# Performance work log

Measured on AMD Instinct MI355X. Metric: run time of the kernel, lower is better.

The kernel has to match this reference:

```python
import jax, jax.numpy as jnp
import numpy as np

EMBED_DIM = 256
NUM_HEADS = 8
HEAD_DIM = EMBED_DIM // NUM_HEADS


def setup_inputs() -> dict:
    key = jax.random.key(0)
    ks = jax.random.split(key, 16)
    B, N, E = 4, 2048, EMBED_DIM
    s = 1.0 / np.sqrt(E)
    inp = {
        "x": jax.random.normal(ks[0], (B, N, E), jnp.float32),
        "influence_matrix": jax.random.uniform(ks[1], (B, N, N), jnp.float32),
        "Wq": jax.random.normal(ks[2], (E, E), jnp.float32) * s,
        "Wk": jax.random.normal(ks[3], (E, E), jnp.float32) * s,
        "Wv": jax.random.normal(ks[4], (E, E), jnp.float32) * s,
        "Wo": jax.random.normal(ks[5], (E, E), jnp.float32) * s,
        "bo": jnp.zeros((E,), jnp.float32),
        "iw1": jnp.array(1.0, jnp.float32),
        "ib1": jnp.array(0.0, jnp.float32),
        "iw2": jnp.array(1.0, jnp.float32),
        "ib2": jnp.array(0.0, jnp.float32),
        "W1": jax.random.normal(ks[6], (E, E), jnp.float32) * s,
        "b1": jnp.zeros((E,), jnp.float32),
        "W2": jax.random.normal(ks[7], (E, E), jnp.float32) * s,
        "b2": jnp.zeros((E,), jnp.float32),
        "g1": jnp.ones((E,), jnp.float32),
        "beta1": jnp.zeros((E,), jnp.float32),
        "g2": jnp.ones((E,), jnp.float32),
        "beta2": jnp.zeros((E,), jnp.float32),
    }
    return inp


def _layer_norm(x, g, b, eps=1e-5):
    mu = jnp.mean(x, axis=-1, keepdims=True)
    var = jnp.var(x, axis=-1, keepdims=True)
    return (x - mu) * jax.lax.rsqrt(var + eps) * g + b


def _attention(x, infl, Wq, Wk, Wv, Wo, bo, iw1, ib1, iw2, ib2):
    B, N, E = x.shape
    H, D = NUM_HEADS, HEAD_DIM
    # torch nn.Linear: y = x @ W.T ; here W is stored as (E, E) used directly.
    q = (x @ Wq).reshape(B, N, H, D)
    k = (x @ Wk).reshape(B, N, H, D)
    v = (x @ Wv).reshape(B, N, H, D)
    scores = jnp.einsum("bqhd,bkhd->bhqk", q, k) / np.sqrt(D)  # [B,H,N,N]
    scores = scores + (iw1 * infl + ib1)[:, None, :, :]
    w = jax.nn.softmax(scores, axis=-1)
    w = w * (iw2 * infl + ib2)[:, None, :, :]
    out = jnp.einsum("bhqk,bkhd->bqhd", w, v).reshape(B, N, E)
    return out @ Wo + bo


def reference(x, influence_matrix, Wq, Wk, Wv, Wo, bo, iw1, ib1, iw2, ib2,
              W1, b1, W2, b2, g1, beta1, g2, beta2):
    h = _attention(_layer_norm(x, g1, beta1), influence_matrix,
                   Wq, Wk, Wv, Wo, bo, iw1, ib1, iw2, ib2) + x
    ffn = jax.nn.relu(_layer_norm(h, g2, beta2) @ W1 + b1) @ W2 + b2
    return ffn + h
```

## Files before the change

### kernel.cpp

```cpp
#include <hip/hip_runtime.h>
#include <hip/hip_bf16.h>

#define B_  4
#define N_  2048
#define E_  256
#define H_  8
#define D_  32
#define QT  32
#define KC  64
#define HPB 4
#define VTP 72
#define PP  72
#define IFP 68
#define LOG2E 1.4426950408889634f

typedef __attribute__((ext_vector_type(8))) short bfx8;
typedef __attribute__((ext_vector_type(4))) float fx4;

__device__ __forceinline__ unsigned short f2bf(float f) {
    unsigned int u = __float_as_uint(f);
    u += 0x7fffu + ((u >> 16) & 1u);
    return (unsigned short)(u >> 16);
}

__device__ __forceinline__ float bf2f(unsigned short u) {
    return __uint_as_float((unsigned int)u << 16);
}

__device__ __forceinline__ unsigned int cvt_pk_bf16(float lo, float hi) {
    unsigned int r;
    asm("v_cvt_pk_bf16_f32 %0, %1, %2" : "=v"(r) : "v"(lo), "v"(hi));
    return r;
}

__global__ __launch_bounds__(256) void prep_w(
    const float* Wa, const float* Wb, const float* Wc,
    const float* Wd, const float* We, const float* Wf,
    unsigned short* Oa, unsigned short* Ob, unsigned short* Oc,
    unsigned short* Od, unsigned short* Oe, unsigned short* Of)
{
    int z = blockIdx.z;
    const float* src = z == 0 ? Wa : z == 1 ? Wb : z == 2 ? Wc
                     : z == 3 ? Wd : z == 4 ? We : Wf;
    unsigned short* dst = z == 0 ? Oa : z == 1 ? Ob : z == 2 ? Oc
                        : z == 3 ? Od : z == 4 ? Oe : Of;
    __shared__ float t[32][33];
    int n0 = blockIdx.x * 32, k0 = blockIdx.y * 32;
    int tx = threadIdx.x & 31, ty = threadIdx.x >> 5;
#pragma unroll
    for (int i = 0; i < 4; i++)
        t[ty + i * 8][tx] = src[(k0 + ty + i * 8) * E_ + n0 + tx];
    __syncthreads();
#pragma unroll
    for (int i = 0; i < 4; i++)
        dst[(n0 + ty + i * 8) * E_ + k0 + tx] = f2bf(t[tx][ty + i * 8]);
}

__global__ __launch_bounds__(256) void ln_kernel(const float* __restrict__ x,
                                                 const float* __restrict__ g,
                                                 const float* __restrict__ be,
                                                 unsigned short* __restrict__ out)
{
    const int w = threadIdx.x >> 6, lane = threadIdx.x & 63;
    const long row = (long)blockIdx.x * 4 + w;
    const float* xr = &x[row * E_];
    float4 v = *(const float4*)&xr[lane * 4];
    float s  = v.x + v.y + v.z + v.w;
    float s2 = v.x * v.x + v.y * v.y + v.z * v.z + v.w * v.w;
#pragma unroll
    for (int off = 32; off; off >>= 1) {
        s  += __shfl_xor(s,  off, 64);
        s2 += __shfl_xor(s2, off, 64);
    }
    float mu  = s * (1.0f / E_);
    float var = s2 * (1.0f / E_) - mu * mu;
    float rstd = rsqrtf(var + 1e-5f);
    float4 gg = *(const float4*)&g[lane * 4];
    float4 bb = *(const float4*)&be[lane * 4];
    float y0 = (v.x - mu) * rstd * gg.x + bb.x;
    float y1 = (v.y - mu) * rstd * gg.y + bb.y;
    float y2 = (v.z - mu) * rstd * gg.z + bb.z;
    float y3 = (v.w - mu) * rstd * gg.w + bb.w;
    uint2 o;
    o.x = cvt_pk_bf16(y0, y1);
    o.y = cvt_pk_bf16(y2, y3);
    *(uint2*)&out[row * E_ + lane * 4] = o;
}

__global__ __launch_bounds__(256) void ln_bf16(const unsigned short* __restrict__ x,
                                               const float* __restrict__ g,
                                               const float* __restrict__ be,
                                               unsigned short* __restrict__ out)
{
    const int w = threadIdx.x >> 6, lane = threadIdx.x & 63;
    const long row = (long)blockIdx.x * 4 + w;
    uint2 u = *(const uint2*)&x[row * E_ + lane * 4];
    float v0 = __uint_as_float(u.x << 16);
    float v1 = __uint_as_float(u.x & 0xffff0000u);
    float v2 = __uint_as_float(u.y << 16);
    float v3 = __uint_as_float(u.y & 0xffff0000u);
    float s  = v0 + v1 + v2 + v3;
    float s2 = v0 * v0 + v1 * v1 + v2 * v2 + v3 * v3;
#pragma unroll
    for (int off = 32; off; off >>= 1) {
        s  += __shfl_xor(s,  off, 64);
        s2 += __shfl_xor(s2, off, 64);
    }
    float mu  = s * (1.0f / E_);
    float var = s2 * (1.0f / E_) - mu * mu;
    float rstd = rsqrtf(var + 1e-5f);
    float4 gg = *(const float4*)&g[lane * 4];
    float4 bb = *(const float4*)&be[lane * 4];
    float y0 = (v0 - mu) * rstd * gg.x + bb.x;
    float y1 = (v1 - mu) * rstd * gg.y + bb.y;
    float y2 = (v2 - mu) * rstd * gg.z + bb.z;
    float y3 = (v3 - mu) * rstd * gg.w + bb.w;
    uint2 o;
    o.x = cvt_pk_bf16(y0, y1);
    o.y = cvt_pk_bf16(y2, y3);
    *(uint2*)&out[row * E_ + lane * 4] = o;
}

__device__ __forceinline__ void gemm_core(
    const unsigned short* __restrict__ A,
    const unsigned short* __restrict__ Wt,
    const float* __restrict__ bias,
    const void* __restrict__ resid, int rbf,
    void* __restrict__ Cv, int relu, int obf, int m0, int n0, int ldC)
{
    __shared__ unsigned short As[64 * 264];
    __shared__ unsigned short Bs[64 * 264];
    int tid = threadIdx.x;

    {
        const unsigned short* Ab = A  + (long)m0 * E_;
        const unsigned short* Bb = Wt + (long)n0 * E_;
        bfx8 va[8], vb[8];
#pragma unroll
        for (int i = 0; i < 8; i++) va[i] = *(const bfx8*)&Ab[(i * 256 + tid) * 8];
#pragma unroll
        for (int i = 0; i < 8; i++) vb[i] = *(const bfx8*)&Bb[(i * 256 + tid) * 8];
#pragma unroll
        for (int i = 0; i < 8; i++) {
            int fo = i * 256 + tid;
            int row = fo >> 5, c8 = fo & 31;
            *(bfx8*)&As[row * 264 + c8 * 8] = va[i];
            *(bfx8*)&Bs[row * 264 + c8 * 8] = vb[i];
        }
    }
    __syncthreads();

    int lane = tid & 63, w = tid >> 6;
    int c = lane & 15, g = lane >> 4;
    int wm = (w >> 1) * 32, wn = (w & 1) * 32;
    fx4 acc[2][2] = {};

#pragma unroll
    for (int ks = 0; ks < 8; ks++) {
        bfx8 a0 = *(const bfx8*)&As[(wm + c)      * 264 + ks * 32 + g * 8];
        bfx8 a1 = *(const bfx8*)&As[(wm + 16 + c) * 264 + ks * 32 + g * 8];
        bfx8 b0 = *(const bfx8*)&Bs[(wn + c)      * 264 + ks * 32 + g * 8];
        bfx8 b1 = *(const bfx8*)&Bs[(wn + 16 + c) * 264 + ks * 32 + g * 8];
        acc[0][0] = __builtin_amdgcn_mfma_f32_16x16x32_bf16(a0, b0, acc[0][0], 0, 0, 0);
        acc[0][1] = __builtin_amdgcn_mfma_f32_16x16x32_bf16(a0, b1, acc[0][1], 0, 0, 0);
        acc[1][0] = __builtin_amdgcn_mfma_f32_16x16x32_bf16(a1, b0, acc[1][0], 0, 0, 0);
        acc[1][1] = __builtin_amdgcn_mfma_f32_16x16x32_bf16(a1, b1, acc[1][1], 0, 0, 0);
    }

#pragma unroll
    for (int fm = 0; fm < 2; fm++)
#pragma unroll
        for (int r = 0; r < 4; r++) {
            int m = m0 + wm + fm * 16 + g * 4 + r;
#pragma unroll
            for (int fn = 0; fn < 2; fn++) {
                int n = n0 + wn + fn * 16 + c;
                float o = acc[fm][fn][r];
                if (bias)  o += bias[n];
                if (relu)  o = fmaxf(o, 0.f);
                if (resid) {
                    float rv = rbf ? bf2f(((const unsigned short*)resid)[(long)m * ldC + n])
                                   : ((const float*)resid)[(long)m * ldC + n];
                    o += rv;
                }
                if (obf) ((unsigned short*)Cv)[(long)m * ldC + n] = f2bf(o);
                else     ((float*)Cv)[(long)m * ldC + n] = o;
            }
        }
}

__global__ __launch_bounds__(256, 2) void gemm_mfma(
    const unsigned short* __restrict__ A,
    const unsigned short* __restrict__ Wt,
    const float* __restrict__ bias,
    const void* __restrict__ resid, int rbf,
    void* __restrict__ Cv, int relu, int obf)
{
    gemm_core(A, Wt, bias, resid, rbf, Cv, relu, obf,
              blockIdx.x * 64, blockIdx.y * 64, E_);
}

__global__ __launch_bounds__(256, 2) void gemm_qkv(
    const unsigned short* __restrict__ A,
    const unsigned short* __restrict__ Wq, unsigned short* __restrict__ qo,
    const unsigned short* __restrict__ Wk, unsigned short* __restrict__ ko,
    const unsigned short* __restrict__ Wv, unsigned short* __restrict__ vto)
{
    int z = blockIdx.z;
    if (z == 2) {
        gemm_core(Wv, A, nullptr, nullptr, 0, vto, 0, 1,
                  blockIdx.y * 64, blockIdx.x * 64, B_ * N_);
    } else {
        const unsigned short* Wt = z == 0 ? Wq : Wk;
        unsigned short*       Cv = z == 0 ? qo : ko;
        gemm_core(A, Wt, nullptr, nullptr, 0, Cv, 0, 1,
                  blockIdx.x * 64, blockIdx.y * 64, E_);
    }
}

__global__ __launch_bounds__(256, 2) void attn_mfma(
    const unsigned short* __restrict__ q,
    const unsigned short* __restrict__ k,
    const unsigned short* __restrict__ vt,
    const float* __restrict__ infl,
    const float* __restrict__ iw1p, const float* __restrict__ ib1p,
    const float* __restrict__ iw2p, const float* __restrict__ ib2p,
    unsigned short* __restrict__ out)
{
    const int bx  = blockIdx.x;
    const int xcd = bx & 7;
    const int b   = xcd >> 1;
    const int hg  = (xcd & 1) * HPB;
    const int q0  = (bx >> 3) * QT;
    const int tid = threadIdx.x;
    const int h    = tid >> 6;
    const int head = hg + h;
    const int lane = tid & 63;
    const int c = lane & 15, g = lane >> 4, g4 = g * 4;

    const float iw1e = iw1p[0] * LOG2E, ib1e = ib1p[0] * LOG2E;
    const float iw2 = iw2p[0], ib2 = ib2p[0];
    const float scale2 = 0.17677669529663687f * LOG2E;

    __shared__ unsigned short vt_lds[HPB][D_][VTP];
    __shared__ unsigned short p_lds[HPB][QT][PP];
    __shared__ unsigned int ab_lds[2][QT][IFP];

    bfx8 qf0 = *(const bfx8*)&q[((long)(b * N_ + q0 +      c)) * E_ + head * D_ + g * 8];
    bfx8 qf1 = *(const bfx8*)&q[((long)(b * N_ + q0 + 16 + c)) * E_ + head * D_ + g * 8];

    const unsigned short* kbase = &k[((long)(b * N_) + c) * E_ + head * D_ + g * 8];
    const long MT = (long)B_ * N_;
    const int vrow = lane >> 3, vcol = (lane & 7) * 8;
    const unsigned short* vtg = &vt[((long)(head * D_ + vrow)) * MT + b * N_ + vcol];

    const int irow = tid >> 3, icol = (tid & 7) * 8;
    const float* ibase = &infl[((long)(b * N_ + q0 + irow)) * N_ + icol];

    fx4 o00 = {0,0,0,0}, o01 = {0,0,0,0}, o10 = {0,0,0,0}, o11 = {0,0,0,0};
    float l0 = 0.f, l1 = 0.f;
    const fx4 zero = {0,0,0,0};
    fx4 st[2][4];

    auto stage_ab = [&](int buf, float4 x0, float4 x1) {
        float xs[8] = {x0.x, x0.y, x0.z, x0.w, x1.x, x1.y, x1.z, x1.w};
        unsigned int u[8];
#pragma unroll
        for (int i = 0; i < 8; i++) {
            float a = fmaf(xs[i], iw1e, ib1e);
            float bb = fmaf(xs[i], iw2, ib2);
            u[i] = cvt_pk_bf16(a, bb);
        }
        uint4 lo = {u[0], u[1], u[2], u[3]};
        uint4 hi = {u[4], u[5], u[6], u[7]};
        *(uint4*)&ab_lds[buf][irow][icol]     = lo;
        *(uint4*)&ab_lds[buf][irow][icol + 4] = hi;
    };

    float4 i00 = *(const float4*)&ibase[0];
    float4 i01 = *(const float4*)&ibase[4];
    float4 fA0 = *(const float4*)&ibase[KC];
    float4 fA1 = *(const float4*)&ibase[KC + 4];
    bfx8 nk0 = *(const bfx8*)(kbase +  0L * E_);
    bfx8 nk1 = *(const bfx8*)(kbase + 16L * E_);
    bfx8 nk2 = *(const bfx8*)(kbase + 32L * E_);
    bfx8 nk3 = *(const bfx8*)(kbase + 48L * E_);
    bfx8 nv0 = *(const bfx8*)(vtg +  0L * MT);
    bfx8 nv1 = *(const bfx8*)(vtg +  8L * MT);
    bfx8 nv2 = *(const bfx8*)(vtg + 16L * MT);
    bfx8 nv3 = *(const bfx8*)(vtg + 24L * MT);
    stage_ab(0, i00, i01);
    __syncthreads();
    __builtin_amdgcn_s_setprio(1);
    st[0][0] = __builtin_amdgcn_mfma_f32_16x16x32_bf16(nk0, qf0, zero, 0, 0, 0);
    st[1][0] = __builtin_amdgcn_mfma_f32_16x16x32_bf16(nk0, qf1, zero, 0, 0, 0);
    st[0][1] = __builtin_amdgcn_mfma_f32_16x16x32_bf16(nk1, qf0, zero, 0, 0, 0);
    st[1][1] = __builtin_amdgcn_mfma_f32_16x16x32_bf16(nk1, qf1, zero, 0, 0, 0);
    st[0][2] = __builtin_amdgcn_mfma_f32_16x16x32_bf16(nk2, qf0, zero, 0, 0, 0);
    st[1][2] = __builtin_amdgcn_mfma_f32_16x16x32_bf16(nk2, qf1, zero, 0, 0, 0);
    st[0][3] = __builtin_amdgcn_mfma_f32_16x16x32_bf16(nk3, qf0, zero, 0, 0, 0);
    st[1][3] = __builtin_amdgcn_mfma_f32_16x16x32_bf16(nk3, qf1, zero, 0, 0, 0);
    __builtin_amdgcn_s_setprio(0);
    {
        *(bfx8*)&vt_lds[h][vrow     ][vcol] = nv0;
        *(bfx8*)&vt_lds[h][vrow +  8][vcol] = nv1;
        *(bfx8*)&vt_lds[h][vrow + 16][vcol] = nv2;
        *(bfx8*)&vt_lds[h][vrow + 24][vcol] = nv3;
    }

    for (int kk = 0; kk < N_; kk += KC) {
        const int cur = (kk >> 6) & 1, nxt = cur ^ 1;
        const int kn  = (kk +     KC) & (N_ - 1);
        const int kn2 = (kk + 2 * KC) & (N_ - 1);

        nv0 = *(const bfx8*)(vtg +  0L * MT + kn);
        nv1 = *(const bfx8*)(vtg +  8L * MT + kn);
        nv2 = *(const bfx8*)(vtg + 16L * MT + kn);
        nv3 = *(const bfx8*)(vtg + 24L * MT + kn);
        nk0 = *(const bfx8*)(kbase + (long)(kn +  0) * E_);
        nk1 = *(const bfx8*)(kbase + (long)(kn + 16) * E_);
        nk2 = *(const bfx8*)(kbase + (long)(kn + 32) * E_);
        nk3 = *(const bfx8*)(kbase + (long)(kn + 48) * E_);
        float4 fN0 = *(const float4*)&ibase[kn2];
        float4 fN1 = *(const float4*)&ibase[kn2 + 4];

        stage_ab(nxt, fA0, fA1);

#pragma unroll
        for (int qs = 0; qs < 2; qs++) {
#pragma unroll
            for (int t = 0; t < 4; t++) {
                uint4 u4 = *(const uint4*)&ab_lds[cur][qs * 16 + c][t * 16 + g4];
                unsigned int uu[4] = {u4.x, u4.y, u4.z, u4.w};
                float pr[4];
#pragma unroll
                for (int r = 0; r < 4; r++) {
                    float a  = __uint_as_float(uu[r] << 16);
                    float bb = __uint_as_float(uu[r] & 0xffff0000u);
                    float s = fmaf(st[qs][t][r], scale2, a);
                    float p = __builtin_amdgcn_exp2f(s);
                    if (qs == 0) l0 += p; else l1 += p;
                    pr[r] = p * bb;
                }
                unsigned int lo = cvt_pk_bf16(pr[0], pr[1]);
                unsigned int hi = cvt_pk_bf16(pr[2], pr[3]);
                *(uint2*)&p_lds[h][qs * 16 + c][t * 16 + g4] = make_uint2(lo, hi);
            }
        }

        __builtin_amdgcn_s_setprio(1);
#pragma unroll
        for (int kh = 0; kh < 2; kh++) {
            bfx8 vf0 = *(const bfx8*)&vt_lds[h][c][g * 8 + kh * 32];
            bfx8 vf1 = *(const bfx8*)&vt_lds[h][16 + c][g * 8 + kh * 32];
            bfx8 pf0 = *(const bfx8*)&p_lds[h][c][g * 8 + kh * 32];
            bfx8 pf1 = *(const bfx8*)&p_lds[h][16 + c][g * 8 + kh * 32];
            o00 = __builtin_amdgcn_mfma_f32_16x16x32_bf16(pf0, vf0, o00, 0, 0, 0);
            o01 = __builtin_amdgcn_mfma_f32_16x16x32_bf16(pf0, vf1, o01, 0, 0, 0);
            o10 = __builtin_amdgcn_mfma_f32_16x16x32_bf16(pf1, vf0, o10, 0, 0, 0);
            o11 = __builtin_amdgcn_mfma_f32_16x16x32_bf16(pf1, vf1, o11, 0, 0, 0);
        }
        __builtin_amdgcn_s_setprio(0);

        __syncthreads();

        if (kk != N_ - KC) {
            __builtin_amdgcn_s_setprio(1);
            st[0][0] = __builtin_amdgcn_mfma_f32_16x16x32_bf16(nk0, qf0, zero, 0, 0, 0);
            st[1][0] = __builtin_amdgcn_mfma_f32_16x16x32_bf16(nk0, qf1, zero, 0, 0, 0);
            st[0][1] = __builtin_amdgcn_mfma_f32_16x16x32_bf16(nk1, qf0, zero, 0, 0, 0);
            st[1][1] = __builtin_amdgcn_mfma_f32_16x16x32_bf16(nk1, qf1, zero, 0, 0, 0);
            st[0][2] = __builtin_amdgcn_mfma_f32_16x16x32_bf16(nk2, qf0, zero, 0, 0, 0);
            st[1][2] = __builtin_amdgcn_mfma_f32_16x16x32_bf16(nk2, qf1, zero, 0, 0, 0);
            st[0][3] = __builtin_amdgcn_mfma_f32_16x16x32_bf16(nk3, qf0, zero, 0, 0, 0);
            st[1][3] = __builtin_amdgcn_mfma_f32_16x16x32_bf16(nk3, qf1, zero, 0, 0, 0);
            __builtin_amdgcn_s_setprio(0);
            *(bfx8*)&vt_lds[h][vrow     ][vcol] = nv0;
            *(bfx8*)&vt_lds[h][vrow +  8][vcol] = nv1;
            *(bfx8*)&vt_lds[h][vrow + 16][vcol] = nv2;
            *(bfx8*)&vt_lds[h][vrow + 24][vcol] = nv3;
        }
        fA0 = fN0; fA1 = fN1;
    }

    float l0r = l0;
    l0r += __shfl_xor(l0r, 16); l0r += __shfl_xor(l0r, 32);
    float l1r = l1;
    l1r += __shfl_xor(l1r, 16); l1r += __shfl_xor(l1r, 32);
#pragma unroll
    for (int r = 0; r < 4; r++) {
        int src = (lane & 48) | (g4 + r);
        float inv0 = 1.0f / __shfl(l0r, src, 64);
        float inv1 = 1.0f / __shfl(l1r, src, 64);
        long row0 = ((long)(b * N_ + q0 +      g4 + r)) * E_ + head * D_;
        long row1 = ((long)(b * N_ + q0 + 16 + g4 + r)) * E_ + head * D_;
        out[row0 + c]      = f2bf(o00[r] * inv0);
        out[row0 + 16 + c] = f2bf(o01[r] * inv0);
        out[row1 + c]      = f2bf(o10[r] * inv1);
        out[row1 + 16 + c] = f2bf(o11[r] * inv1);
    }
}

extern "C" void kernel_launch(void* const* d_in, const int* in_sizes, int n_in,
                              void* d_out, int out_size, void* d_ws, size_t ws_size,
                              hipStream_t stream)
{
    (void)in_sizes; (void)n_in; (void)out_size; (void)ws_size;
    const float* x    = (const float*)d_in[0];
    const float* infl = (const float*)d_in[1];
    const float* Wq   = (const float*)d_in[2];
    const float* Wk   = (const float*)d_in[3];
    const float* Wv   = (const float*)d_in[4];
    const float* Wo   = (const float*)d_in[5];
    const float* bo   = (const float*)d_in[6];
    const float* iw1  = (const float*)d_in[7];
    const float* ib1  = (const float*)d_in[8];
    const float* iw2  = (const float*)d_in[9];
    const float* ib2  = (const float*)d_in[10];
    const float* W1   = (const float*)d_in[11];
    const float* b1   = (const float*)d_in[12];
    const float* W2   = (const float*)d_in[13];
    const float* b2   = (const float*)d_in[14];
    const float* g1   = (const float*)d_in[15];
    const float* be1  = (const float*)d_in[16];
    const float* g2   = (const float*)d_in[17];
    const float* be2  = (const float*)d_in[18];

    char* base = (char*)d_ws;
    unsigned short* hb  = (unsigned short*)base;
    unsigned short* lnb = (unsigned short*)(base + (4  << 20));
    unsigned short* qb  = (unsigned short*)(base + (8  << 20));
    unsigned short* kb  = (unsigned short*)(base + (12 << 20));
    unsigned short* vtb = (unsigned short*)(base + (16 << 20));
    unsigned short* wqt = (unsigned short*)(base + (20 << 20));
    unsigned short* wkt = wqt + 65536;
    unsigned short* wvt = wkt + 65536;
    unsigned short* wot = wvt + 65536;
    unsigned short* w1t = wot + 65536;
    unsigned short* w2t = w1t + 65536;

    dim3 gemm_grid(128, 4);

    prep_w<<<dim3(8, 8, 6), 256, 0, stream>>>(Wq, Wk, Wv, Wo, W1, W2,
                                              wqt, wkt, wvt, wot, w1t, w2t);
    ln_kernel<<<B_ * N_ / 4, 256, 0, stream>>>(x, g1, be1, lnb);
    gemm_qkv<<<dim3(128, 4, 3), 256, 0, stream>>>(lnb, wqt, qb, wkt, kb, wvt, vtb);
    attn_mfma<<<B_ * (N_ / QT) * 2, 256, 0, stream>>>(qb, kb, vtb, infl,
                                                      iw1, ib1, iw2, ib2, lnb);
    gemm_mfma<<<gemm_grid, 256, 0, stream>>>(lnb, wot, bo, x, 0, hb, 0, 1);
    ln_bf16<<<B_ * N_ / 4, 256, 0, stream>>>(hb, g2, be2, lnb);
    gemm_mfma<<<gemm_grid, 256, 0, stream>>>(lnb, w1t, b1, nullptr, 0, qb, 1, 1);
    gemm_mfma<<<gemm_grid, 256, 0, stream>>>(qb, w2t, b2, hb, 1, (float*)d_out, 0, 0);
}
```

Before: 124.3 us.

## Split attention blocks into two heads each with 128 threads

Halves heads per attention block (4 to 2), launching twice as many 128-thread blocks with occupancy hint 4. The influence-tile staging is widened so 128 threads each load 16 values per row chunk. This aims to raise parallelism and occupancy but makes each influence tile be read and converted by twice as many blocks, relying on cache to absorb the redundant traffic.

```diff
diff --git a/kernel.cpp b/kernel.cpp
--- a/kernel.cpp
+++ b/kernel.cpp
@@ -8,7 +8,7 @@
 #define D_  32
 #define QT  32
 #define KC  64
-#define HPB 4
+#define HPB 2
 #define VTP 72
 #define PP  72
 #define IFP 68
@@ -218,7 +218,7 @@
     }
 }
 
-__global__ __launch_bounds__(256, 2) void attn_mfma(
+__global__ __launch_bounds__(128, 4) void attn_mfma(
     const unsigned short* __restrict__ q,
     const unsigned short* __restrict__ k,
     const unsigned short* __restrict__ vt,
@@ -227,11 +227,11 @@
     const float* __restrict__ iw2p, const float* __restrict__ ib2p,
     unsigned short* __restrict__ out)
 {
-    const int bx  = blockIdx.x;
-    const int xcd = bx & 7;
-    const int b   = xcd >> 1;
-    const int hg  = (xcd & 1) * HPB;
-    const int q0  = (bx >> 3) * QT;
+    const int bx    = blockIdx.x;
+    const int group = bx & 15;
+    const int b     = group >> 2;
+    const int hg    = (group & 3) * HPB;
+    const int q0    = (bx >> 4) * QT;
     const int tid = threadIdx.x;
     const int h    = tid >> 6;
     const int head = hg + h;
@@ -254,7 +254,7 @@
     const int vrow = lane >> 3, vcol = (lane & 7) * 8;
     const unsigned short* vtg = &vt[((long)(head * D_ + vrow)) * MT + b * N_ + vcol];
 
-    const int irow = tid >> 3, icol = (tid & 7) * 8;
+    const int irow = tid >> 2, icol = (tid & 3) * 16;
     const float* ibase = &infl[((long)(b * N_ + q0 + irow)) * N_ + icol];
 
     fx4 o00 = {0,0,0,0}, o01 = {0,0,0,0}, o10 = {0,0,0,0}, o11 = {0,0,0,0};
@@ -262,25 +262,31 @@
     const fx4 zero = {0,0,0,0};
     fx4 st[2][4];
 
-    auto stage_ab = [&](int buf, float4 x0, float4 x1) {
-        float xs[8] = {x0.x, x0.y, x0.z, x0.w, x1.x, x1.y, x1.z, x1.w};
-        unsigned int u[8];
-#pragma unroll
-        for (int i = 0; i < 8; i++) {
-            float a = fmaf(xs[i], iw1e, ib1e);
+    auto stage_ab = [&](int buf, float4 x0, float4 x1, float4 x2, float4 x3) {
+        float xs[16] = {x0.x, x0.y, x0.z, x0.w, x1.x, x1.y, x1.z, x1.w,
+                        x2.x, x2.y, x2.z, x2.w, x3.x, x3.y, x3.z, x3.w};
+        unsigned int u[16];
+#pragma unroll
+        for (int i = 0; i < 16; i++) {
+            float a  = fmaf(xs[i], iw1e, ib1e);
             float bb = fmaf(xs[i], iw2, ib2);
             u[i] = cvt_pk_bf16(a, bb);
         }
-        uint4 lo = {u[0], u[1], u[2], u[3]};
-        uint4 hi = {u[4], u[5], u[6], u[7]};
-        *(uint4*)&ab_lds[buf][irow][icol]     = lo;
-        *(uint4*)&ab_lds[buf][irow][icol + 4] = hi;
+#pragma unroll
+        for (int j = 0; j < 4; j++) {
+            uint4 w4 = {u[j * 4], u[j * 4 + 1], u[j * 4 + 2], u[j * 4 + 3]};
+            *(uint4*)&ab_lds[buf][irow][icol + j * 4] = w4;
+        }
     };
 
-    float4 i00 = *(const float4*)&ibase[0];
-    float4 i01 = *(const float4*)&ibase[4];
+    float4 i0 = *(const float4*)&ibase[0];
+    float4 i1 = *(const float4*)&ibase[4];
+    float4 i2 = *(const float4*)&ibase[8];
+    float4 i3 = *(const float4*)&ibase[12];
     float4 fA0 = *(const float4*)&ibase[KC];
     float4 fA1 = *(const float4*)&ibase[KC + 4];
+    float4 fA2 = *(const float4*)&ibase[KC + 8];
+    float4 fA3 = *(const float4*)&ibase[KC + 12];
     bfx8 nk0 = *(const bfx8*)(kbase +  0L * E_);
     bfx8 nk1 = *(const bfx8*)(kbase + 16L * E_);
     bfx8 nk2 = *(const bfx8*)(kbase + 32L * E_);
@@ -289,7 +295,7 @@
     bfx8 nv1 = *(const bfx8*)(vtg +  8L * MT);
     bfx8 nv2 = *(const bfx8*)(vtg + 16L * MT);
     bfx8 nv3 = *(const bfx8*)(vtg + 24L * MT);
-    stage_ab(0, i00, i01);
+    stage_ab(0, i0, i1, i2, i3);
     __syncthreads();
     __builtin_amdgcn_s_setprio(1);
     st[0][0] = __builtin_amdgcn_mfma_f32_16x16x32_bf16(nk0, qf0, zero, 0, 0, 0);
@@ -323,8 +329,10 @@
         nk3 = *(const bfx8*)(kbase + (long)(kn + 48) * E_);
         float4 fN0 = *(const float4*)&ibase[kn2];
         float4 fN1 = *(const float4*)&ibase[kn2 + 4];
-
-        stage_ab(nxt, fA0, fA1);
+        float4 fN2 = *(const float4*)&ibase[kn2 + 8];
+        float4 fN3 = *(const float4*)&ibase[kn2 + 12];
+
+        stage_ab(nxt, fA0, fA1, fA2, fA3);
 
 #pragma unroll
         for (int qs = 0; qs < 2; qs++) {
@@ -380,7 +388,7 @@
             *(bfx8*)&vt_lds[h][vrow + 16][vcol] = nv2;
             *(bfx8*)&vt_lds[h][vrow + 24][vcol] = nv3;
         }
-        fA0 = fN0; fA1 = fN1;
+        fA0 = fN0; fA1 = fN1; fA2 = fN2; fA3 = fN3;
     }
 
     float l0r = l0;
@@ -445,8 +453,8 @@
                                               wqt, wkt, wvt, wot, w1t, w2t);
     ln_kernel<<<B_ * N_ / 4, 256, 0, stream>>>(x, g1, be1, lnb);
     gemm_qkv<<<dim3(128, 4, 3), 256, 0, stream>>>(lnb, wqt, qb, wkt, kb, wvt, vtb);
-    attn_mfma<<<B_ * (N_ / QT) * 2, 256, 0, stream>>>(qb, kb, vtb, infl,
-                                                      iw1, ib1, iw2, ib2, lnb);
+    attn_mfma<<<B_ * (N_ / QT) * (H_ / HPB), 128, 0, stream>>>(qb, kb, vtb, infl,
+                                                    iw1, ib1, iw2, ib2, lnb);
     gemm_mfma<<<gemm_grid, 256, 0, stream>>>(lnb, wot, bo, x, 0, hb, 0, 1);
     ln_bf16<<<B_ * N_ / 4, 256, 0, stream>>>(hb, g2, be2, lnb);
     gemm_mfma<<<gemm_grid, 256, 0, stream>>>(lnb, w1t, b1, nullptr, 0, qb, 1, 1);
```

New measurement: 134.6 us. +8.3%, slower.

## Split attention key range across two blocks and add combine kernel

Applied to the files above, without the earlier changes.

Splits each attention block's key loop into two halves handled by separate blocks, doubling the grid. Each half writes unnormalized fp32 partial outputs and row sums to workspace, and a new combine kernel sums them, normalizes, and converts to bf16. This aims to raise parallelism and latency hiding, at the cost of extra fp32 partial traffic and an additional launch. It relies on the softmax using no per-split running max, so partials can simply be added.

```diff
diff --git a/kernel.cpp b/kernel.cpp
--- a/kernel.cpp
+++ b/kernel.cpp
@@ -9,6 +9,7 @@
 #define QT  32
 #define KC  64
 #define HPB 4
+#define KS  2
 #define VTP 72
 #define PP  72
 #define IFP 68
@@ -225,13 +226,17 @@
     const float* __restrict__ infl,
     const float* __restrict__ iw1p, const float* __restrict__ ib1p,
     const float* __restrict__ iw2p, const float* __restrict__ ib2p,
-    unsigned short* __restrict__ out)
+    float* __restrict__ opart,
+    float* __restrict__ lpart)
 {
     const int bx  = blockIdx.x;
     const int xcd = bx & 7;
     const int b   = xcd >> 1;
     const int hg  = (xcd & 1) * HPB;
-    const int q0  = (bx >> 3) * QT;
+    const int ks  = (bx >> 3) & 1;
+    const int q0  = (bx >> 4) * QT;
+    const int kof = ks * (N_ / 2);
+    const int NH  = N_ / 2;
     const int tid = threadIdx.x;
     const int h    = tid >> 6;
     const int head = hg + h;
@@ -277,18 +282,18 @@
         *(uint4*)&ab_lds[buf][irow][icol + 4] = hi;
     };
 
-    float4 i00 = *(const float4*)&ibase[0];
-    float4 i01 = *(const float4*)&ibase[4];
-    float4 fA0 = *(const float4*)&ibase[KC];
-    float4 fA1 = *(const float4*)&ibase[KC + 4];
-    bfx8 nk0 = *(const bfx8*)(kbase +  0L * E_);
-    bfx8 nk1 = *(const bfx8*)(kbase + 16L * E_);
-    bfx8 nk2 = *(const bfx8*)(kbase + 32L * E_);
-    bfx8 nk3 = *(const bfx8*)(kbase + 48L * E_);
-    bfx8 nv0 = *(const bfx8*)(vtg +  0L * MT);
-    bfx8 nv1 = *(const bfx8*)(vtg +  8L * MT);
-    bfx8 nv2 = *(const bfx8*)(vtg + 16L * MT);
-    bfx8 nv3 = *(const bfx8*)(vtg + 24L * MT);
+    float4 i00 = *(const float4*)&ibase[kof];
+    float4 i01 = *(const float4*)&ibase[kof + 4];
+    float4 fA0 = *(const float4*)&ibase[kof + KC];
+    float4 fA1 = *(const float4*)&ibase[kof + KC + 4];
+    bfx8 nk0 = *(const bfx8*)(kbase + (long)(kof +  0) * E_);
+    bfx8 nk1 = *(const bfx8*)(kbase + (long)(kof + 16) * E_);
+    bfx8 nk2 = *(const bfx8*)(kbase + (long)(kof + 32) * E_);
+    bfx8 nk3 = *(const bfx8*)(kbase + (long)(kof + 48) * E_);
+    bfx8 nv0 = *(const bfx8*)(vtg +  0L * MT + kof);
+    bfx8 nv1 = *(const bfx8*)(vtg +  8L * MT + kof);
+    bfx8 nv2 = *(const bfx8*)(vtg + 16L * MT + kof);
+    bfx8 nv3 = *(const bfx8*)(vtg + 24L * MT + kof);
     stage_ab(0, i00, i01);
     __syncthreads();
     __builtin_amdgcn_s_setprio(1);
@@ -308,10 +313,10 @@
         *(bfx8*)&vt_lds[h][vrow + 24][vcol] = nv3;
     }
 
-    for (int kk = 0; kk < N_; kk += KC) {
+    for (int kk = 0; kk < NH; kk += KC) {
         const int cur = (kk >> 6) & 1, nxt = cur ^ 1;
-        const int kn  = (kk +     KC) & (N_ - 1);
-        const int kn2 = (kk + 2 * KC) & (N_ - 1);
+        const int kn  = kof + ((kk +     KC) & (NH - 1));
+        const int kn2 = kof + ((kk + 2 * KC) & (NH - 1));
 
         nv0 = *(const bfx8*)(vtg +  0L * MT + kn);
         nv1 = *(const bfx8*)(vtg +  8L * MT + kn);
@@ -364,7 +369,7 @@
 
         __syncthreads();
 
-        if (kk != N_ - KC) {
+        if (kk != NH - KC) {
             __builtin_amdgcn_s_setprio(1);
             st[0][0] = __builtin_amdgcn_mfma_f32_16x16x32_bf16(nk0, qf0, zero, 0, 0, 0);
             st[1][0] = __builtin_amdgcn_mfma_f32_16x16x32_bf16(nk0, qf1, zero, 0, 0, 0);
@@ -387,18 +392,44 @@
     l0r += __shfl_xor(l0r, 16); l0r += __shfl_xor(l0r, 32);
     float l1r = l1;
     l1r += __shfl_xor(l1r, 16); l1r += __shfl_xor(l1r, 32);
+    const long SZ = (long)B_ * N_ * E_;
+    float* op = opart + (long)ks * SZ;
 #pragma unroll
     for (int r = 0; r < 4; r++) {
-        int src = (lane & 48) | (g4 + r);
-        float inv0 = 1.0f / __shfl(l0r, src, 64);
-        float inv1 = 1.0f / __shfl(l1r, src, 64);
         long row0 = ((long)(b * N_ + q0 +      g4 + r)) * E_ + head * D_;
         long row1 = ((long)(b * N_ + q0 + 16 + g4 + r)) * E_ + head * D_;
-        out[row0 + c]      = f2bf(o00[r] * inv0);
-        out[row0 + 16 + c] = f2bf(o01[r] * inv0);
-        out[row1 + c]      = f2bf(o10[r] * inv1);
-        out[row1 + 16 + c] = f2bf(o11[r] * inv1);
-    }
+        op[row0 + c]      = o00[r];
+        op[row0 + 16 + c] = o01[r];
+        op[row1 + c]      = o10[r];
+        op[row1 + 16 + c] = o11[r];
+    }
+    if (g == 0) {
+        long lb = (((long)ks * B_ + b) * H_ + head) * N_ + q0;
+        lpart[lb + c]      = l0r;
+        lpart[lb + 16 + c] = l1r;
+    }
+}
+
+__global__ __launch_bounds__(256) void attn_combine(
+    const float* __restrict__ opart, const float* __restrict__ lpart,
+    unsigned short* __restrict__ out)
+{
+    const int w = threadIdx.x >> 6, lane = threadIdx.x & 63;
+    const long row = (long)blockIdx.x * 4 + w;
+    const int b = (int)(row >> 11);
+    const int n = (int)(row & (N_ - 1));
+    const int d = lane * 4;
+    const int h = d >> 5;
+    const long SZ = (long)B_ * N_ * E_;
+    float4 o0 = *(const float4*)&opart[row * E_ + d];
+    float4 o1 = *(const float4*)&opart[SZ + row * E_ + d];
+    float l = lpart[((long)(b * H_ + h)) * N_ + n]
+            + lpart[((long)((B_ + b) * H_ + h)) * N_ + n];
+    float inv = 1.0f / l;
+    uint2 o;
+    o.x = cvt_pk_bf16((o0.x + o1.x) * inv, (o0.y + o1.y) * inv);
+    o.y = cvt_pk_bf16((o0.z + o1.z) * inv, (o0.w + o1.w) * inv);
+    *(uint2*)&out[row * E_ + d] = o;
 }
 
 extern "C" void kernel_launch(void* const* d_in, const int* in_sizes, int n_in,
@@ -438,6 +469,8 @@
     unsigned short* wot = wvt + 65536;
     unsigned short* w1t = wot + 65536;
     unsigned short* w2t = w1t + 65536;
+    float* opart = (float*)(base + (21 << 20));
+    float* lpart = (float*)(base + (37 << 20));
 
     dim3 gemm_grid(128, 4);
 
@@ -445,8 +478,9 @@
                                               wqt, wkt, wvt, wot, w1t, w2t);
     ln_kernel<<<B_ * N_ / 4, 256, 0, stream>>>(x, g1, be1, lnb);
     gemm_qkv<<<dim3(128, 4, 3), 256, 0, stream>>>(lnb, wqt, qb, wkt, kb, wvt, vtb);
-    attn_mfma<<<B_ * (N_ / QT) * 2, 256, 0, stream>>>(qb, kb, vtb, infl,
-                                                      iw1, ib1, iw2, ib2, lnb);
+    attn_mfma<<<B_ * (N_ / QT) * 2 * KS, 256, 0, stream>>>(qb, kb, vtb, infl,
+                                        iw1, ib1, iw2, ib2, opart, lpart);
+    attn_combine<<<B_ * N_ / 4, 256, 0, stream>>>(opart, lpart, lnb);
     gemm_mfma<<<gemm_grid, 256, 0, stream>>>(lnb, wot, bo, x, 0, hb, 0, 1);
     ln_bf16<<<B_ * N_ / 4, 256, 0, stream>>>(hb, g2, be2, lnb);
     gemm_mfma<<<gemm_grid, 256, 0, stream>>>(lnb, w1t, b1, nullptr, 0, qb, 1, 1);
```

Result: slower. 130.7 us (+5.1%).
